# Optimization experiments

Hardware: AMD Instinct MI355X
Metric: run time of the kernel (lower is better)

Reference implementation:

```python
import jax, jax.numpy as jnp
import numpy as np

LENGTHSCALE = 1.0  # heat-kernel time parameter of the spectral measure


def setup_inputs() -> dict:
    key = jax.random.key(0)
    k1, k2, k3, k4 = jax.random.split(key, 4)
    N, M, L, D = 4096, 4096, 512, 3
    x = jax.random.normal(k1, (N, D), dtype=jnp.float32)
    y = jax.random.normal(k2, (M, D), dtype=jnp.float32)
    freqs = jax.random.normal(k3, (L, D), dtype=jnp.float32)
    lb_eigenvalues = jax.random.uniform(k4, (L,), dtype=jnp.float32)
    variance = jnp.ones((1,), dtype=jnp.float32)
    return {"x": x, "y": y, "freqs": freqs,
            "lb_eigenvalues": lb_eigenvalues, "variance": variance}


def reference(x, y, freqs, lb_eigenvalues, variance):
    # spectral measure weights w_l = measure(lmd_l) = exp(-t/2 * lmd_l)
    w = jnp.exp(-0.5 * LENGTHSCALE * lb_eigenvalues)           # [L]
    # phase_function_l(x_n - y_m) = exp(i <f_l, x_n - y_m>); real part is
    # cos(<f_l,x_n> - <f_l,y_m>) = cos px cos py + sin px sin py, which turns
    # the loop-sum over eigenspaces into two GEMMs (fused accumulation).
    px = x @ freqs.T                                           # [N, L]
    py = y @ freqs.T                                           # [M, L]
    cov = (jnp.cos(px) * w) @ jnp.cos(py).T + (jnp.sin(px) * w) @ jnp.sin(py).T
    # normalizer = forward(p, p, normalize=False)[0, 0] = sum_l w_l * cos(0)
    normalizer = jnp.sum(w)
    return jnp.abs(variance[0]) * cov / normalizer
```

## Files before the change

### kernel.cpp

```cpp
#include <hip/hip_runtime.h>
#include <hip/hip_bf16.h>
#include <math.h>

#define NDIM 4096
#define MDIM 4096
#define LDIM 512
#define KDIM 1024

typedef float f32x4 __attribute__((ext_vector_type(4)));

__device__ __align__(16) unsigned long long g_At[(size_t)128 * NDIM];
__device__ __align__(16) unsigned long long g_Bt[(size_t)128 * MDIM];

__global__ __launch_bounds__(512) void scale_kernel(const float* __restrict__ lam,
                                                    const float* __restrict__ var,
                                                    float* __restrict__ ws) {
  int l = threadIdx.x;
  float v = expf(-0.5f * lam[l]);
  #pragma unroll
  for (int off = 32; off > 0; off >>= 1) v += __shfl_down(v, off, 64);
  __shared__ float red[8];
  if ((l & 63) == 0) red[l >> 6] = v;
  __syncthreads();
  if (l == 0) {
    float t = 0.f;
    #pragma unroll
    for (int i = 0; i < 8; ++i) t += red[i];
    ws[0] = fabsf(var[0]) / t;
  }
}

__global__ __launch_bounds__(256) void phase_kernel(const float* __restrict__ x,
                                                    const float* __restrict__ y,
                                                    const float* __restrict__ freqs,
                                                    const float* __restrict__ lam) {
  int tid = threadIdx.x;
  int blk = blockIdx.x;
  int p = (blk & 127) * 64 + (tid & 63);
  int o = (blk >> 7) * 4 + (tid >> 6);
  bool isA = (p < NDIM);
  int rr = isA ? p : (p - NDIM);
  const float* pt = (isA ? x : y) + 3 * (size_t)rr;
  float p0 = pt[0], p1 = pt[1], p2 = pt[2];

  float cv[8], sv[8];
  #pragma unroll
  for (int i = 0; i < 8; ++i) {
    int li = o * 8 + i;
    float px = p0 * freqs[3 * li] + p1 * freqs[3 * li + 1] + p2 * freqs[3 * li + 2];
    float sn, cs;
    __sincosf(px, &sn, &cs);
    float wl = isA ? expf(-0.5f * lam[li]) : 1.0f;
    cv[i] = cs * wl;
    sv[i] = sn * wl;
  }
  union { int i2[2]; unsigned long long u; } pc, ps;
  pc.i2[0] = __builtin_amdgcn_cvt_pk_fp8_f32(cv[0], cv[1], 0, 0);
  pc.i2[0] = __builtin_amdgcn_cvt_pk_fp8_f32(cv[2], cv[3], pc.i2[0], 1);
  pc.i2[1] = __builtin_amdgcn_cvt_pk_fp8_f32(cv[4], cv[5], 0, 0);
  pc.i2[1] = __builtin_amdgcn_cvt_pk_fp8_f32(cv[6], cv[7], pc.i2[1], 1);
  ps.i2[0] = __builtin_amdgcn_cvt_pk_fp8_f32(sv[0], sv[1], 0, 0);
  ps.i2[0] = __builtin_amdgcn_cvt_pk_fp8_f32(sv[2], sv[3], ps.i2[0], 1);
  ps.i2[1] = __builtin_amdgcn_cvt_pk_fp8_f32(sv[4], sv[5], 0, 0);
  ps.i2[1] = __builtin_amdgcn_cvt_pk_fp8_f32(sv[6], sv[7], ps.i2[1], 1);

  unsigned long long* base = (isA ? g_At : g_Bt) + rr;
  base[(size_t)o * NDIM]        = pc.u;
  base[(size_t)(o + 64) * NDIM] = ps.u;
}

__global__ __launch_bounds__(512, 2) void gemm_kernel(float* __restrict__ C,
                                                      const float* __restrict__ ws) {
  int bid = blockIdx.x;
  int xcd = bid & 7;
  int slt = bid >> 3;
  int sup = 2 * xcd + (slt >> 4);
  int w_  = slt & 15;
  int brow = ((sup >> 2) * 4 + (w_ >> 2)) * 256;
  int bcol = ((sup & 3) * 4 + (w_ & 3)) * 256;

  int tid  = threadIdx.x;
  int lane = tid & 63;
  int wid  = tid >> 6;
  int wm   = wid >> 2;
  int wn   = wid & 3;
  int fr   = lane & 15;
  int oct  = lane >> 4;

  float s_val = ws[0];

  const unsigned long long* At = g_At + (size_t)oct * NDIM + (brow + wm * 128 + fr);
  const unsigned long long* Bt = g_Bt + (size_t)oct * MDIM + (bcol + wn * 64 + fr);

  f32x4 acc[8][4] = {};
  long pa0, pa1, pa2, pa3, pa4, pa5, pa6, pa7, pb0, pb1, pb2, pb3;
  long qa0, qa1, qa2, qa3, qa4, qa5, qa6, qa7, qb0, qb1, qb2, qb3;

#define LOADH(S, H)                                                          \
  { const unsigned long long* Ap_ = At + (size_t)(H) * 4 * NDIM;             \
    const unsigned long long* Bp_ = Bt + (size_t)(H) * 4 * MDIM;             \
    S##a0 = (long)Ap_[0];   S##a1 = (long)Ap_[16];                           \
    S##a2 = (long)Ap_[32];  S##a3 = (long)Ap_[48];                           \
    S##a4 = (long)Ap_[64];  S##a5 = (long)Ap_[80];                           \
    S##a6 = (long)Ap_[96];  S##a7 = (long)Ap_[112];                          \
    S##b0 = (long)Bp_[0];   S##b1 = (long)Bp_[16];                           \
    S##b2 = (long)Bp_[32];  S##b3 = (long)Bp_[48]; }

#define MFH1(M, AF, S)                                                       \
  acc[M][0] = __builtin_amdgcn_mfma_f32_16x16x32_fp8_fp8(AF, S##b0, acc[M][0], 0, 0, 0); \
  acc[M][1] = __builtin_amdgcn_mfma_f32_16x16x32_fp8_fp8(AF, S##b1, acc[M][1], 0, 0, 0); \
  acc[M][2] = __builtin_amdgcn_mfma_f32_16x16x32_fp8_fp8(AF, S##b2, acc[M][2], 0, 0, 0); \
  acc[M][3] = __builtin_amdgcn_mfma_f32_16x16x32_fp8_fp8(AF, S##b3, acc[M][3], 0, 0, 0);

#define MFH(S)                                                               \
  MFH1(0, S##a0, S) MFH1(1, S##a1, S) MFH1(2, S##a2, S) MFH1(3, S##a3, S)    \
  MFH1(4, S##a4, S) MFH1(5, S##a5, S) MFH1(6, S##a6, S) MFH1(7, S##a7, S)

  LOADH(p, 0);
  for (int hh = 0; hh < 15; ++hh) {
    LOADH(q, 2 * hh + 1);
    MFH(p);
    LOADH(p, 2 * hh + 2);
    MFH(q);
  }
  LOADH(q, 31);
  MFH(p);
  MFH(q);

  int crow = brow + wm * 128 + (lane >> 4) * 4;
  int ccol = bcol + wn * 64 + (lane & 15);
  #pragma unroll
  for (int mi = 0; mi < 8; ++mi)
    #pragma unroll
    for (int n = 0; n < 4; ++n)
      #pragma unroll
      for (int j = 0; j < 4; ++j)
        C[(size_t)(crow + mi * 16 + j) * MDIM + (ccol + n * 16)] = s_val * acc[mi][n][j];
}

extern "C" void kernel_launch(void* const* d_in, const int* in_sizes, int n_in,
                              void* d_out, int out_size, void* d_ws, size_t ws_size,
                              hipStream_t stream) {
  const float* x     = (const float*)d_in[0];
  const float* y     = (const float*)d_in[1];
  const float* freqs = (const float*)d_in[2];
  const float* lam   = (const float*)d_in[3];
  const float* var   = (const float*)d_in[4];
  float* out = (float*)d_out;
  float* ws  = (float*)d_ws;

  hipLaunchKernelGGL(scale_kernel, dim3(1), dim3(512), 0, stream, lam, var, ws);
  hipLaunchKernelGGL(phase_kernel, dim3(2048), dim3(256), 0, stream,
                     x, y, freqs, lam);
  hipLaunchKernelGGL(gemm_kernel, dim3((NDIM / 256) * (MDIM / 256)), dim3(512), 0, stream,
                     out, ws);
}
```

Baseline: 54.28 us.

## Stage A operand through LDS with async global-to-LDS loads and software pipeline

The GEMM now stages the A tile (shared by the 4 wn-warps) into a double-buffered LDS region using global_load_lds, with an XOR swizzle to avoid bank conflicts. B stays in direct global register loads. Explicit vmcnt/lgkmcnt waits, sched barriers, and setprio around MFMA blocks build a manual pipeline. This cuts redundant global/L2 traffic for A, at the cost of barriers per half-step and fragile hand-tuned wait counts.

```diff
diff --git a/kernel.cpp b/kernel.cpp
--- a/kernel.cpp
+++ b/kernel.cpp
@@ -11,6 +11,13 @@
 
 __device__ __align__(16) unsigned long long g_At[(size_t)128 * NDIM];
 __device__ __align__(16) unsigned long long g_Bt[(size_t)128 * MDIM];
+
+#define GLOBAL_AS __attribute__((address_space(1)))
+#define LDS_AS __attribute__((address_space(3)))
+
+__device__ __forceinline__ void gload_lds16(void* lds, const void* g) {
+  __builtin_amdgcn_global_load_lds((const GLOBAL_AS void*)g, (LDS_AS void*)lds, 16, 0, 0);
+}
 
 __global__ __launch_bounds__(512) void scale_kernel(const float* __restrict__ lam,
                                                     const float* __restrict__ var,
@@ -71,6 +78,8 @@
 
 __global__ __launch_bounds__(512, 2) void gemm_kernel(float* __restrict__ C,
                                                       const float* __restrict__ ws) {
+  __shared__ __align__(16) unsigned long long Asl[2][2][1024];
+
   int bid = blockIdx.x;
   int xcd = bid & 7;
   int slt = bid >> 3;
@@ -89,43 +98,114 @@
 
   float s_val = ws[0];
 
-  const unsigned long long* At = g_At + (size_t)oct * NDIM + (brow + wm * 128 + fr);
+  int aoff = oct * 2048 + ((fr ^ (oct << 2)) << 3) + wm * 1024;
+
+  int so  = tid >> 7;
+  int si  = tid & 127;
+  const unsigned long long* gAsrc =
+      g_At + (size_t)so * NDIM + brow + ((2 * si) ^ (so << 2));
+
   const unsigned long long* Bt = g_Bt + (size_t)oct * MDIM + (bcol + wn * 64 + fr);
 
   f32x4 acc[8][4] = {};
-  long pa0, pa1, pa2, pa3, pa4, pa5, pa6, pa7, pb0, pb1, pb2, pb3;
-  long qa0, qa1, qa2, qa3, qa4, qa5, qa6, qa7, qb0, qb1, qb2, qb3;
-
-#define LOADH(S, H)                                                          \
-  { const unsigned long long* Ap_ = At + (size_t)(H) * 4 * NDIM;             \
-    const unsigned long long* Bp_ = Bt + (size_t)(H) * 4 * MDIM;             \
-    S##a0 = (long)Ap_[0];   S##a1 = (long)Ap_[16];                           \
-    S##a2 = (long)Ap_[32];  S##a3 = (long)Ap_[48];                           \
-    S##a4 = (long)Ap_[64];  S##a5 = (long)Ap_[80];                           \
-    S##a6 = (long)Ap_[96];  S##a7 = (long)Ap_[112];                          \
-    S##b0 = (long)Bp_[0];   S##b1 = (long)Bp_[16];                           \
-    S##b2 = (long)Bp_[32];  S##b3 = (long)Bp_[48]; }
-
-#define MFH1(M, AF, S)                                                       \
-  acc[M][0] = __builtin_amdgcn_mfma_f32_16x16x32_fp8_fp8(AF, S##b0, acc[M][0], 0, 0, 0); \
-  acc[M][1] = __builtin_amdgcn_mfma_f32_16x16x32_fp8_fp8(AF, S##b1, acc[M][1], 0, 0, 0); \
-  acc[M][2] = __builtin_amdgcn_mfma_f32_16x16x32_fp8_fp8(AF, S##b2, acc[M][2], 0, 0, 0); \
-  acc[M][3] = __builtin_amdgcn_mfma_f32_16x16x32_fp8_fp8(AF, S##b3, acc[M][3], 0, 0, 0);
-
-#define MFH(S)                                                               \
-  MFH1(0, S##a0, S) MFH1(1, S##a1, S) MFH1(2, S##a2, S) MFH1(3, S##a3, S)    \
-  MFH1(4, S##a4, S) MFH1(5, S##a5, S) MFH1(6, S##a6, S) MFH1(7, S##a7, S)
-
-  LOADH(p, 0);
-  for (int hh = 0; hh < 15; ++hh) {
-    LOADH(q, 2 * hh + 1);
-    MFH(p);
-    LOADH(p, 2 * hh + 2);
-    MFH(q);
-  }
-  LOADH(q, 31);
-  MFH(p);
-  MFH(q);
+  long s0_0, s0_1, s0_2, s0_3, s0_4, s0_5, s0_6, s0_7;
+  long s1_0, s1_1, s1_2, s1_3, s1_4, s1_5, s1_6, s1_7;
+  long u0, u1, u2, u3;
+  long v0, v1, v2, v3;
+
+#define STAGE(T1, KK)                                                        \
+  {                                                                          \
+    char* d_ = (char*)&Asl[(T1) & 1][(KK)][0] + tid * 16;                    \
+    const unsigned long long* s_ = gAsrc + (size_t)((T1) * 8 + (KK) * 4) * NDIM; \
+    gload_lds16(d_, s_);                                                     \
+  }
+
+#define VMCNT(N) asm volatile("s_waitcnt vmcnt(" #N ")" ::: "memory")
+#define LGKM(N)  asm volatile("s_waitcnt lgkmcnt(" #N ")" ::: "memory")
+#define SCHED0   __builtin_amdgcn_sched_barrier(0)
+#define BAR      __builtin_amdgcn_s_barrier()
+
+#define AREAD(S, T, KK)                                                      \
+  { const char* Ab_ = (const char*)&Asl[(T) & 1][(KK)][0] + aoff;            \
+    S##0 = *(const long*)(Ab_ + 0 * 128);                                    \
+    S##1 = *(const long*)(Ab_ + 1 * 128);                                    \
+    S##2 = *(const long*)(Ab_ + 2 * 128);                                    \
+    S##3 = *(const long*)(Ab_ + 3 * 128);                                    \
+    S##4 = *(const long*)(Ab_ + 4 * 128);                                    \
+    S##5 = *(const long*)(Ab_ + 5 * 128);                                    \
+    S##6 = *(const long*)(Ab_ + 6 * 128);                                    \
+    S##7 = *(const long*)(Ab_ + 7 * 128); }
+
+#define BGLOB(B0, B1, B2, B3, T, KK)                                         \
+  { const unsigned long long* p_ = Bt + (size_t)((T) * 8 + (KK) * 4) * MDIM; \
+    B0 = (long)p_[0];                                                        \
+    B1 = (long)p_[16];                                                       \
+    B2 = (long)p_[32];                                                       \
+    B3 = (long)p_[48]; }
+
+#define MFMA4(I, AF, B0, B1, B2, B3)                                                   \
+  acc[I][0] = __builtin_amdgcn_mfma_f32_16x16x32_fp8_fp8(AF, B0, acc[I][0], 0, 0, 0);  \
+  acc[I][1] = __builtin_amdgcn_mfma_f32_16x16x32_fp8_fp8(AF, B1, acc[I][1], 0, 0, 0);  \
+  acc[I][2] = __builtin_amdgcn_mfma_f32_16x16x32_fp8_fp8(AF, B2, acc[I][2], 0, 0, 0);  \
+  acc[I][3] = __builtin_amdgcn_mfma_f32_16x16x32_fp8_fp8(AF, B3, acc[I][3], 0, 0, 0);
+
+#define MFMA32(S, B0, B1, B2, B3)                                            \
+  __builtin_amdgcn_s_setprio(1);                                             \
+  MFMA4(0, S##0, B0, B1, B2, B3) MFMA4(1, S##1, B0, B1, B2, B3)              \
+  MFMA4(2, S##2, B0, B1, B2, B3) MFMA4(3, S##3, B0, B1, B2, B3)              \
+  MFMA4(4, S##4, B0, B1, B2, B3) MFMA4(5, S##5, B0, B1, B2, B3)              \
+  MFMA4(6, S##6, B0, B1, B2, B3) MFMA4(7, S##7, B0, B1, B2, B3)              \
+  __builtin_amdgcn_s_setprio(0);
+
+  STAGE(0, 0);
+  STAGE(0, 1);
+  STAGE(1, 0);
+  BGLOB(u0, u1, u2, u3, 0, 0);
+  SCHED0;
+  VMCNT(5);
+  BAR;
+  AREAD(s0_, 0, 0);
+
+  for (int t = 0; t < 14; ++t) {
+    AREAD(s1_, t, 1);
+    BGLOB(v0, v1, v2, v3, t, 1);
+    SCHED0;
+    LGKM(8); SCHED0;
+    MFMA32(s0_, u0, u1, u2, u3);
+    STAGE(t + 1, 1);
+    VMCNT(5);
+    BAR;
+    AREAD(s0_, t + 1, 0);
+    BGLOB(u0, u1, u2, u3, t + 1, 0);
+    SCHED0;
+    LGKM(8); SCHED0;
+    MFMA32(s1_, v0, v1, v2, v3);
+    STAGE(t + 2, 0);
+    VMCNT(5);
+    BAR;
+  }
+  AREAD(s1_, 14, 1);
+  BGLOB(v0, v1, v2, v3, 14, 1);
+  SCHED0;
+  LGKM(8); SCHED0;
+  MFMA32(s0_, u0, u1, u2, u3);
+  STAGE(15, 1);
+  VMCNT(5);
+  BAR;
+  AREAD(s0_, 15, 0);
+  BGLOB(u0, u1, u2, u3, 15, 0);
+  SCHED0;
+  LGKM(8); SCHED0;
+  MFMA32(s1_, v0, v1, v2, v3);
+  VMCNT(4);
+  BAR;
+  AREAD(s1_, 15, 1);
+  BGLOB(v0, v1, v2, v3, 15, 1);
+  SCHED0;
+  LGKM(8); SCHED0;
+  MFMA32(s0_, u0, u1, u2, u3);
+  LGKM(0); SCHED0;
+  MFMA32(s1_, v0, v1, v2, v3);
 
   int crow = brow + wm * 128 + (lane >> 4) * 4;
   int ccol = bcol + wn * 64 + (lane & 15);
```

New measurement: 55.72 us. 2.7% more time.
